# Kernel tuning notes

Measured on AMD Instinct MI355X. Metric: run time of the kernel, lower is better.

The kernel has to match this reference:

```python
import jax, jax.numpy as jnp
import numpy as np

NUM_RELATIONS = 8


def rgcn_conv(x, edge_index, edge_type, W, root, bias):
    """PyG RGCNConv (full weights, aggr='mean'): for each relation r, mean-aggregate
    W_r @ x_src over incoming edges of type r at each target node, sum over relations,
    then add root transform and bias."""
    N = x.shape[0]
    src, dst = edge_index[0], edge_index[1]
    # per-(relation, dst) edge counts for mean aggregation
    comb = edge_type * N + dst  # [E]
    cnt = jax.ops.segment_sum(jnp.ones(src.shape[0], x.dtype), comb,
                              num_segments=NUM_RELATIONS * N)  # [R*N]
    inv = jnp.where(cnt > 0, 1.0 / cnt, 0.0)
    # per-relation transformed features [R, N, H]
    xW = jnp.einsum('ni,rio->rno', x, W)
    # per-edge message, pre-scaled by 1/count for mean aggregation
    msg = xW[edge_type, src] * inv[comb][:, None]  # [E, H]
    agg = jax.ops.segment_sum(msg, dst, num_segments=N)  # [N, H]
    return agg + x @ root + bias


def setup_inputs() -> dict:
    key = jax.random.key(0)
    ks = jax.random.split(key, 9)
    N, E, D, H, C, R = 50000, 600000, 128, 128, 16, NUM_RELATIONS
    s1 = 1.0 / np.sqrt(D)
    s2 = 1.0 / np.sqrt(H)
    return {
        'x': jax.random.normal(ks[0], (N, D), jnp.float32),
        'edge_index': jax.random.randint(ks[1], (2, E), 0, N, jnp.int32),
        'edge_type': jax.random.randint(ks[2], (E,), 0, R, jnp.int32),
        'W1': jax.random.normal(ks[3], (R, D, H), jnp.float32) * s1,
        'root1': jax.random.normal(ks[4], (D, H), jnp.float32) * s1,
        'b1': jnp.zeros((H,), jnp.float32),
        'W2': jax.random.normal(ks[5], (R, H, H), jnp.float32) * s2,
        'root2': jax.random.normal(ks[6], (H, H), jnp.float32) * s2,
        'b2': jnp.zeros((H,), jnp.float32),
        'Wc': jax.random.normal(ks[7], (H, C), jnp.float32) * s2,
        'bc': jnp.zeros((C,), jnp.float32),
    }


def reference(x, edge_index, edge_type, W1, root1, b1, W2, root2, b2, Wc, bc):
    h = jax.nn.relu(rgcn_conv(x, edge_index, edge_type, W1, root1, b1))
    # dropout(p=0.2) is identity in eval mode
    embeddings = rgcn_conv(h, edge_index, edge_type, W2, root2, b2)
    out = embeddings @ Wc + bc
    return (out, embeddings)
```

## Files before the change

kernel.cpp:

```cpp
#include <hip/hip_runtime.h>

#define NREL 8

typedef __attribute__((ext_vector_type(8))) short bf16x8;
typedef __attribute__((ext_vector_type(4))) float f32x4;

__device__ inline ushort f2bf(float f)
{
    union { float f; unsigned u; } v; v.f = f;
    unsigned r = v.u + 0x7FFF + ((v.u >> 16) & 1);
    return (ushort)(r >> 16);
}

__device__ inline unsigned cvtpk(float lo, float hi)
{
    unsigned r;
    asm("v_cvt_pk_bf16_f32 %0, %1, %2" : "=v"(r) : "v"(lo), "v"(hi));
    return r;
}

__global__ __launch_bounds__(256) void prep1(
    float4* __restrict__ cntz, int cnt4,
    const float* __restrict__ x, ushort* __restrict__ xb, int nx4,
    const float* __restrict__ W1, const float* __restrict__ root1,
    ushort* __restrict__ Wf1,
    const float* __restrict__ W2, const float* __restrict__ root2,
    ushort* __restrict__ Wf2)
{
    int tid = blockIdx.x * 256 + threadIdx.x;
    int stride = gridDim.x * 256;

    for (int i = tid; i < cnt4; i += stride)
        cntz[i] = make_float4(0.f, 0.f, 0.f, 0.f);

    for (int i = tid; i < nx4; i += stride) {
        float4 v = ((const float4*)x)[i];
        ushort4 o;
        o.x = f2bf(v.x); o.y = f2bf(v.y); o.z = f2bf(v.z); o.w = f2bf(v.w);
        ((ushort4*)xb)[i] = o;
    }

    const int WFN = 128 * 1152;
    for (int i = tid; i < 2 * WFN; i += stride) {
        int half = (i >= WFN);
        int j = half ? i - WFN : i;
        const float* W    = half ? W2 : W1;
        const float* root = half ? root2 : root1;
        ushort* Wf        = half ? Wf2 : Wf1;
        int f = j >> 9;
        int within = j & 511;
        int l = within >> 3;
        int jj = within & 7;
        int rs = f >> 5;
        int kk = (f >> 3) & 3;
        int n  = f & 7;
        int col = (n << 4) | (l & 15);
        int kl  = kk * 32 + (l >> 4) * 8 + jj;
        float v = (rs < 8) ? W[rs * 16384 + kl * 128 + col]
                           : root[kl * 128 + col];
        Wf[j] = f2bf(v);
    }
}

__global__ __launch_bounds__(256) void count_edges(
    const int* __restrict__ ei, const int* __restrict__ et,
    int* __restrict__ cnt, int E, int N)
{
    int e = blockIdx.x * 256 + threadIdx.x;
    if (e < E) {
        int d = ei[E + e];
        int r = et[e];
        atomicAdd(&cnt[r * N + d], 1);
    }
}

__global__ __launch_bounds__(256) void scan1f(
    const int* __restrict__ cnt, float* __restrict__ invc8,
    int* __restrict__ part, int* __restrict__ bsum, int N)
{
    __shared__ int tmp[256];
    int d = blockIdx.x * 256 + threadIdx.x;
    int s = 0;
    if (d < N) {
        #pragma unroll
        for (int r = 0; r < NREL; r++) {
            int c = cnt[r * N + d];
            s += c;
            invc8[(size_t)d * 8 + r] = (c > 0) ? 1.f / (float)c : 0.f;
        }
    }
    int v = s;
    tmp[threadIdx.x] = v;
    __syncthreads();
    for (int off = 1; off < 256; off <<= 1) {
        int t = (threadIdx.x >= off) ? tmp[threadIdx.x - off] : 0;
        __syncthreads();
        tmp[threadIdx.x] += t;
        __syncthreads();
    }
    if (d < N) part[d] = tmp[threadIdx.x] - v;
    if (threadIdx.x == 255) bsum[blockIdx.x] = tmp[255];
}

__global__ __launch_bounds__(1024) void scan2(int* __restrict__ bsum, int nb)
{
    __shared__ int tmp[1024];
    int tid = threadIdx.x;
    int v = (tid < nb) ? bsum[tid] : 0;
    tmp[tid] = v;
    __syncthreads();
    for (int off = 1; off < 1024; off <<= 1) {
        int t = (tid >= off) ? tmp[tid - off] : 0;
        __syncthreads();
        tmp[tid] += t;
        __syncthreads();
    }
    if (tid < nb) bsum[tid] = tmp[tid] - v;
}

__global__ __launch_bounds__(256) void scan3(
    const int* __restrict__ part, const int* __restrict__ bsum,
    int* __restrict__ rowptr, int* __restrict__ cursor, int n, int E)
{
    int i = blockIdx.x * 256 + threadIdx.x;
    if (i < n) {
        int v = part[i] + bsum[blockIdx.x];
        rowptr[i] = v;
        cursor[i] = v;
    }
    if (i == 0) rowptr[n] = E;
}

__global__ __launch_bounds__(256) void fill_csr(
    const int* __restrict__ ei, const int* __restrict__ et,
    int* __restrict__ cursor, int* __restrict__ spk, int E)
{
    int e = blockIdx.x * 256 + threadIdx.x;
    if (e < E) {
        int d = ei[E + e];
        int pos = atomicAdd(&cursor[d], 1);
        spk[pos] = (ei[e] << 8) | et[e];
    }
}

__global__ __launch_bounds__(1024, 8) void fused_layer(
    const ushort* __restrict__ Xb, const int* __restrict__ rowptr,
    const int* __restrict__ spk, const float* __restrict__ invc8,
    const ushort* __restrict__ Wf, const float* __restrict__ bias,
    float* __restrict__ Ofp, ushort* __restrict__ Obf,
    const float* __restrict__ Wc, const float* __restrict__ bc,
    float* __restrict__ outC, int N, int relu)
{
    __shared__ ushort lds[8 * 32 * 128];
    __shared__ f32x4 pscr[2][512];

    int wid  = threadIdx.x >> 6;
    int lane = threadIdx.x & 63;
    int blk0 = blockIdx.x * 32;
    int lane4 = lane << 2;

    #pragma unroll 1
    for (int rr = 0; rr < 2; rr++) {
        int lrow32 = wid * 2 + rr;
        int d = blk0 + lrow32;

        float2 a0 = {0.f, 0.f}, a1 = {0.f, 0.f}, a2 = {0.f, 0.f}, a3 = {0.f, 0.f};
        float2 a4 = {0.f, 0.f}, a5 = {0.f, 0.f}, a6 = {0.f, 0.f}, a7 = {0.f, 0.f};

        #define ROWLD(SP) \
            (*(const unsigned*)((const char*)Xb + (unsigned)((SP) | lane4)))
        #define CONSUME(P, U)                                               \
        {                                                                   \
            union { unsigned u; float f; } lo, hi;                          \
            lo.u = (U) << 16; hi.u = (U) & 0xFFFF0000u;                     \
            switch ((P) & 0xFF) {                                           \
                case 0: a0.x += lo.f; a0.y += hi.f; break;                  \
                case 1: a1.x += lo.f; a1.y += hi.f; break;                  \
                case 2: a2.x += lo.f; a2.y += hi.f; break;                  \
                case 3: a3.x += lo.f; a3.y += hi.f; break;                  \
                case 4: a4.x += lo.f; a4.y += hi.f; break;                  \
                case 5: a5.x += lo.f; a5.y += hi.f; break;                  \
                case 6: a6.x += lo.f; a6.y += hi.f; break;                  \
                default: a7.x += lo.f; a7.y += hi.f; break;                 \
            }                                                               \
        }

        if (d < N) {
            int beg = rowptr[d], end = rowptr[d + 1];
            int i = beg;
            int pk8 = (i + 8 <= end) ? spk[i + (lane & 7)] : 0;
            for (; i + 8 <= end; ) {
                int cur = pk8;
                i += 8;
                if (i + 8 <= end) pk8 = spk[i + (lane & 7)];
                int p0 = __builtin_amdgcn_readlane(cur, 0);
                int p1 = __builtin_amdgcn_readlane(cur, 1);
                int p2 = __builtin_amdgcn_readlane(cur, 2);
                int p3 = __builtin_amdgcn_readlane(cur, 3);
                int p4 = __builtin_amdgcn_readlane(cur, 4);
                int p5 = __builtin_amdgcn_readlane(cur, 5);
                int p6 = __builtin_amdgcn_readlane(cur, 6);
                int p7 = __builtin_amdgcn_readlane(cur, 7);
                unsigned u0 = ROWLD(p0 & 0xFFFFFF00);
                unsigned u1 = ROWLD(p1 & 0xFFFFFF00);
                unsigned u2 = ROWLD(p2 & 0xFFFFFF00);
                unsigned u3 = ROWLD(p3 & 0xFFFFFF00);
                unsigned u4 = ROWLD(p4 & 0xFFFFFF00);
                unsigned u5 = ROWLD(p5 & 0xFFFFFF00);
                unsigned u6 = ROWLD(p6 & 0xFFFFFF00);
                unsigned u7 = ROWLD(p7 & 0xFFFFFF00);
                CONSUME(p0, u0);
                CONSUME(p1, u1);
                CONSUME(p2, u2);
                CONSUME(p3, u3);
                CONSUME(p4, u4);
                CONSUME(p5, u5);
                CONSUME(p6, u6);
                CONSUME(p7, u7);
            }
            for (; i + 4 <= end; i += 4) {
                int pk4 = spk[i + (lane & 3)];
                int p0 = __builtin_amdgcn_readlane(pk4, 0);
                int p1 = __builtin_amdgcn_readlane(pk4, 1);
                int p2 = __builtin_amdgcn_readlane(pk4, 2);
                int p3 = __builtin_amdgcn_readlane(pk4, 3);
                unsigned u0 = ROWLD(p0 & 0xFFFFFF00);
                unsigned u1 = ROWLD(p1 & 0xFFFFFF00);
                unsigned u2 = ROWLD(p2 & 0xFFFFFF00);
                unsigned u3 = ROWLD(p3 & 0xFFFFFF00);
                CONSUME(p0, u0);
                CONSUME(p1, u1);
                CONSUME(p2, u2);
                CONSUME(p3, u3);
            }
            for (; i < end; i++) {
                int p = __builtin_amdgcn_readfirstlane(spk[i]);
                unsigned u = ROWLD(p & 0xFFFFFF00);
                CONSUME(p, u);
            }
        }
        #undef CONSUME
        #undef ROWLD

        f32x4 iv0 = {0.f, 0.f, 0.f, 0.f}, iv1 = {0.f, 0.f, 0.f, 0.f};
        if (d < N) {
            iv0 = *(const f32x4*)&invc8[(size_t)d * 8];
            iv1 = *(const f32x4*)&invc8[(size_t)d * 8 + 4];
        }
        unsigned swz = (unsigned)(lrow32 & 7) << 4;
        char* rowbase = (char*)lds + (lrow32 << 8);
        unsigned wroff = (((unsigned)lane << 2)) ^ swz;
        #define WR2(R, A, IV)                                               \
        {                                                                   \
            unsigned pk = cvtpk(A.x * (IV), A.y * (IV));                    \
            *(unsigned*)(rowbase + (R << 13) + wroff) = pk;                 \
        }
        WR2(0, a0, iv0[0]) WR2(1, a1, iv0[1]) WR2(2, a2, iv0[2]) WR2(3, a3, iv0[3])
        WR2(4, a4, iv1[0]) WR2(5, a5, iv1[1]) WR2(6, a6, iv1[2]) WR2(7, a7, iv1[3])
        #undef WR2
    }
    __syncthreads();

    int lrow = lane & 15;
    int kgrp = lane >> 4;
    unsigned swzR = (unsigned)(lrow & 7) << 4;
    const bf16x8* Wf8 = (const bf16x8*)Wf;
    int n0    = wid & 7;
    int upper = wid >> 3;

    f32x4 acc0 = {0.f, 0.f, 0.f, 0.f};
    f32x4 acc1 = {0.f, 0.f, 0.f, 0.f};
    const char* ldsb = (const char*)lds;

    int rs0 = upper * 4;
    #pragma unroll 1
    for (int rs = rs0; rs < rs0 + 4; rs++) {
        const bf16x8* Bp = Wf8 + (size_t)rs * 2048 + (size_t)n0 * 64 + lane;
        bf16x8 b0 = Bp[0];
        bf16x8 b1 = Bp[512];
        bf16x8 b2 = Bp[1024];
        bf16x8 b3 = Bp[1536];
        const char* ab0 = ldsb + (rs << 13) + ((0 + lrow) << 8);
        const char* ab1 = ldsb + (rs << 13) + ((16 + lrow) << 8);
        {
            bf16x8 a0 = *(const bf16x8*)(ab0 + ((unsigned)(0 * 64 + kgrp * 16) ^ swzR));
            bf16x8 a1 = *(const bf16x8*)(ab0 + ((unsigned)(1 * 64 + kgrp * 16) ^ swzR));
            bf16x8 a2 = *(const bf16x8*)(ab0 + ((unsigned)(2 * 64 + kgrp * 16) ^ swzR));
            bf16x8 a3 = *(const bf16x8*)(ab0 + ((unsigned)(3 * 64 + kgrp * 16) ^ swzR));
            acc0 = __builtin_amdgcn_mfma_f32_16x16x32_bf16(a0, b0, acc0, 0, 0, 0);
            acc0 = __builtin_amdgcn_mfma_f32_16x16x32_bf16(a1, b1, acc0, 0, 0, 0);
            acc0 = __builtin_amdgcn_mfma_f32_16x16x32_bf16(a2, b2, acc0, 0, 0, 0);
            acc0 = __builtin_amdgcn_mfma_f32_16x16x32_bf16(a3, b3, acc0, 0, 0, 0);
        }
        {
            bf16x8 a0 = *(const bf16x8*)(ab1 + ((unsigned)(0 * 64 + kgrp * 16) ^ swzR));
            bf16x8 a1 = *(const bf16x8*)(ab1 + ((unsigned)(1 * 64 + kgrp * 16) ^ swzR));
            bf16x8 a2 = *(const bf16x8*)(ab1 + ((unsigned)(2 * 64 + kgrp * 16) ^ swzR));
            bf16x8 a3 = *(const bf16x8*)(ab1 + ((unsigned)(3 * 64 + kgrp * 16) ^ swzR));
            acc1 = __builtin_amdgcn_mfma_f32_16x16x32_bf16(a0, b0, acc1, 0, 0, 0);
            acc1 = __builtin_amdgcn_mfma_f32_16x16x32_bf16(a1, b1, acc1, 0, 0, 0);
            acc1 = __builtin_amdgcn_mfma_f32_16x16x32_bf16(a2, b2, acc1, 0, 0, 0);
            acc1 = __builtin_amdgcn_mfma_f32_16x16x32_bf16(a3, b3, acc1, 0, 0, 0);
        }
    }
    {
        int arow0 = blk0 + lrow;      if (arow0 >= N) arow0 = N - 1;
        int arow1 = blk0 + 16 + lrow; if (arow1 >= N) arow1 = N - 1;
        const ushort* A0 = Xb + (size_t)arow0 * 128;
        const ushort* A1 = Xb + (size_t)arow1 * 128;
        const bf16x8* Bp = Wf8 + (size_t)8 * 2048 + (size_t)n0 * 64 + lane;
        int kkb = upper * 2;
        bf16x8 b0 = Bp[(kkb + 0) * 512];
        bf16x8 b1 = Bp[(kkb + 1) * 512];
        bf16x8 a00 = *(const bf16x8*)(A0 + (kkb + 0) * 32 + kgrp * 8);
        bf16x8 a01 = *(const bf16x8*)(A0 + (kkb + 1) * 32 + kgrp * 8);
        bf16x8 a10 = *(const bf16x8*)(A1 + (kkb + 0) * 32 + kgrp * 8);
        bf16x8 a11 = *(const bf16x8*)(A1 + (kkb + 1) * 32 + kgrp * 8);
        acc0 = __builtin_amdgcn_mfma_f32_16x16x32_bf16(a00, b0, acc0, 0, 0, 0);
        acc0 = __builtin_amdgcn_mfma_f32_16x16x32_bf16(a01, b1, acc0, 0, 0, 0);
        acc1 = __builtin_amdgcn_mfma_f32_16x16x32_bf16(a10, b0, acc1, 0, 0, 0);
        acc1 = __builtin_amdgcn_mfma_f32_16x16x32_bf16(a11, b1, acc1, 0, 0, 0);
    }

    if (upper) {
        pscr[0][n0 * 64 + lane] = acc0;
        pscr[1][n0 * 64 + lane] = acc1;
    }
    __syncthreads();

    if (!upper) {
        f32x4 p0 = pscr[0][n0 * 64 + lane];
        f32x4 p1 = pscr[1][n0 * 64 + lane];
        int col = n0 * 16 + lrow;
        float bv = bias[col];
        float* embt = (float*)lds;
        #pragma unroll
        for (int rg = 0; rg < 2; rg++) {
            int lrowb = rg * 16 + kgrp * 4;
            f32x4 a = rg ? acc1 : acc0;
            f32x4 pp = rg ? p1 : p0;
            #pragma unroll
            for (int r = 0; r < 4; r++) {
                int row = blk0 + lrowb + r;
                float v = a[r] + pp[r] + bv;
                if (relu) v = fmaxf(v, 0.f);
                if (outC) embt[(lrowb + r) * 128 + col] = v;
                if (row < N) {
                    if (Ofp) Ofp[(size_t)row * 128 + col] = v;
                    if (Obf) Obf[(size_t)row * 128 + col] = f2bf(v);
                }
            }
        }
    }

    if (outC) {
        __syncthreads();
        int t = threadIdx.x;
        if (t < 512) {
            int row = t >> 4;
            int c = t & 15;
            const float* er = (const float*)lds + row * 128;
            float acc2 = bc[c];
            #pragma unroll 8
            for (int k = 0; k < 128; k++) acc2 += er[k] * Wc[k * 16 + c];
            int grow = blk0 + row;
            if (grow < N) outC[(size_t)grow * 16 + c] = acc2;
        }
    }
}

static inline size_t align256(size_t x) { return (x + 255) & ~(size_t)255; }

extern "C" void kernel_launch(void* const* d_in, const int* in_sizes, int n_in,
                              void* d_out, int out_size, void* d_ws, size_t ws_size,
                              hipStream_t stream)
{
    const float* x     = (const float*)d_in[0];
    const int*   ei    = (const int*)d_in[1];
    const int*   et    = (const int*)d_in[2];
    const float* W1    = (const float*)d_in[3];
    const float* root1 = (const float*)d_in[4];
    const float* b1    = (const float*)d_in[5];
    const float* W2    = (const float*)d_in[6];
    const float* root2 = (const float*)d_in[7];
    const float* b2    = (const float*)d_in[8];
    const float* Wc    = (const float*)d_in[9];
    const float* bc    = (const float*)d_in[10];

    const int N = in_sizes[0] / 128;
    const int E = in_sizes[2];
    const int C = in_sizes[10];

    float* out = (float*)d_out;
    float* emb = out + (size_t)N * C;

    size_t cntB  = align256((size_t)NREL * N * sizeof(int));
    size_t rpB   = align256((size_t)(N + 1) * sizeof(int));
    size_t curB  = align256((size_t)N * sizeof(int));
    size_t bsB   = align256((size_t)1024 * sizeof(int));
    size_t invB  = align256((size_t)N * 8 * sizeof(float));
    size_t spkB  = align256((size_t)E * sizeof(int));
    size_t xbB   = align256((size_t)N * 128 * sizeof(ushort));
    size_t wtB   = align256((size_t)128 * 1152 * sizeof(ushort));

    char* p = (char*)d_ws;
    int*    cnt    = (int*)p;      p += cntB;
    int*    rowptr = (int*)p;      p += rpB;
    int*    cursor = (int*)p;      p += curB;
    int*    part   = (int*)p;      p += curB;
    int*    bsum   = (int*)p;      p += bsB;
    float*  invc8  = (float*)p;    p += invB;
    int*    spk    = (int*)p;      p += spkB;
    ushort* xb     = (ushort*)p;   p += xbB;
    ushort* hb     = (ushort*)p;   p += xbB;
    ushort* Wf1    = (ushort*)p;   p += wtB;
    ushort* Wf2    = (ushort*)p;

    dim3 blk(256);
    int gE    = (E + 255) / 256;
    int gN    = (N + 255) / 256;
    int gFus  = (N + 31) / 32;
    long long cnt4 = (long long)NREL * N / 4;
    int nx4 = N * 32;

    prep1<<<2048, blk, 0, stream>>>((float4*)cnt, (int)cnt4,
                                    x, xb, nx4,
                                    W1, root1, Wf1, W2, root2, Wf2);

    count_edges<<<gE, blk, 0, stream>>>(ei, et, cnt, E, N);
    scan1f<<<gN, blk, 0, stream>>>(cnt, invc8, part, bsum, N);
    scan2<<<1, 1024, 0, stream>>>(bsum, gN);
    scan3<<<gN, blk, 0, stream>>>(part, bsum, rowptr, cursor, N, E);
    fill_csr<<<gE, blk, 0, stream>>>(ei, et, cursor, spk, E);

    fused_layer<<<gFus, dim3(1024), 0, stream>>>(
        xb, rowptr, spk, invc8, Wf1, b1, nullptr, hb,
        nullptr, nullptr, nullptr, N, 1);

    fused_layer<<<gFus, dim3(1024), 0, stream>>>(
        hb, rowptr, spk, invc8, Wf2, b2, emb, nullptr,
        Wc, bc, out, N, 0);
}
```

Before: 236.4 us.

## Sort nodes by in-degree to balance work across waves in fused layer

Builds a degree histogram, scans it, and fills a permutation that groups destination nodes by in-degree. The fused layer kernels process nodes in that permuted order, so the waves within a block see similar edge counts and idle less. The change also drops the software prefetch of the next packed-edge chunk and pads the LDS embedding stride to 132 floats to avoid bank conflicts. In exchange it adds three small kernel launches, an extra indirection per row, and scattered output writes.

New measurement: 570.4 us. 141% more time.

```diff
diff --git a/kernel.cpp b/kernel.cpp
--- a/kernel.cpp
+++ b/kernel.cpp
@@ -20,7 +20,7 @@
 }
 
 __global__ __launch_bounds__(256) void prep1(
-    float4* __restrict__ cntz, int cnt4,
+    float4* __restrict__ cntz, int cnt4, int* __restrict__ hist,
     const float* __restrict__ x, ushort* __restrict__ xb, int nx4,
     const float* __restrict__ W1, const float* __restrict__ root1,
     ushort* __restrict__ Wf1,
@@ -32,6 +32,7 @@
 
     for (int i = tid; i < cnt4; i += stride)
         cntz[i] = make_float4(0.f, 0.f, 0.f, 0.f);
+    if (tid < 512) hist[tid] = 0;
 
     for (int i = tid; i < nx4; i += stride) {
         float4 v = ((const float4*)x)[i];
@@ -143,9 +144,50 @@
     }
 }
 
+__global__ __launch_bounds__(256) void deg_hist(
+    const int* __restrict__ rowptr, int* __restrict__ hist, int N)
+{
+    int d = blockIdx.x * 256 + threadIdx.x;
+    if (d < N) {
+        int deg = rowptr[d + 1] - rowptr[d];
+        if (deg > 511) deg = 511;
+        atomicAdd(&hist[deg], 1);
+    }
+}
+
+__global__ __launch_bounds__(512) void hist_scan(int* __restrict__ hist)
+{
+    __shared__ int tmp[512];
+    int tid = threadIdx.x;
+    int v = hist[tid];
+    tmp[tid] = v;
+    __syncthreads();
+    for (int off = 1; off < 512; off <<= 1) {
+        int t = (tid >= off) ? tmp[tid - off] : 0;
+        __syncthreads();
+        tmp[tid] += t;
+        __syncthreads();
+    }
+    hist[tid] = tmp[tid] - v;
+}
+
+__global__ __launch_bounds__(256) void perm_fill(
+    const int* __restrict__ rowptr, int* __restrict__ bincur,
+    int* __restrict__ perm, int N)
+{
+    int d = blockIdx.x * 256 + threadIdx.x;
+    if (d < N) {
+        int deg = rowptr[d + 1] - rowptr[d];
+        if (deg > 511) deg = 511;
+        int pos = atomicAdd(&bincur[deg], 1);
+        perm[pos] = d;
+    }
+}
+
 __global__ __launch_bounds__(1024, 8) void fused_layer(
     const ushort* __restrict__ Xb, const int* __restrict__ rowptr,
     const int* __restrict__ spk, const float* __restrict__ invc8,
+    const int* __restrict__ perm,
     const ushort* __restrict__ Wf, const float* __restrict__ bias,
     float* __restrict__ Ofp, ushort* __restrict__ Obf,
     const float* __restrict__ Wc, const float* __restrict__ bc,
@@ -162,7 +204,8 @@
     #pragma unroll 1
     for (int rr = 0; rr < 2; rr++) {
         int lrow32 = wid * 2 + rr;
-        int d = blk0 + lrow32;
+        int idx = blk0 + lrow32;
+        int d = (idx < N) ? perm[idx] : -1;
 
         float2 a0 = {0.f, 0.f}, a1 = {0.f, 0.f}, a2 = {0.f, 0.f}, a3 = {0.f, 0.f};
         float2 a4 = {0.f, 0.f}, a5 = {0.f, 0.f}, a6 = {0.f, 0.f}, a7 = {0.f, 0.f};
@@ -185,22 +228,19 @@
             }                                                               \
         }
 
-        if (d < N) {
+        if (d >= 0) {
             int beg = rowptr[d], end = rowptr[d + 1];
             int i = beg;
-            int pk8 = (i + 8 <= end) ? spk[i + (lane & 7)] : 0;
-            for (; i + 8 <= end; ) {
-                int cur = pk8;
-                i += 8;
-                if (i + 8 <= end) pk8 = spk[i + (lane & 7)];
-                int p0 = __builtin_amdgcn_readlane(cur, 0);
-                int p1 = __builtin_amdgcn_readlane(cur, 1);
-                int p2 = __builtin_amdgcn_readlane(cur, 2);
-                int p3 = __builtin_amdgcn_readlane(cur, 3);
-                int p4 = __builtin_amdgcn_readlane(cur, 4);
-                int p5 = __builtin_amdgcn_readlane(cur, 5);
-                int p6 = __builtin_amdgcn_readlane(cur, 6);
-                int p7 = __builtin_amdgcn_readlane(cur, 7);
+            for (; i + 8 <= end; i += 8) {
+                int pk8 = spk[i + (lane & 7)];
+                int p0 = __builtin_amdgcn_readlane(pk8, 0);
+                int p1 = __builtin_amdgcn_readlane(pk8, 1);
+                int p2 = __builtin_amdgcn_readlane(pk8, 2);
+                int p3 = __builtin_amdgcn_readlane(pk8, 3);
+                int p4 = __builtin_amdgcn_readlane(pk8, 4);
+                int p5 = __builtin_amdgcn_readlane(pk8, 5);
+                int p6 = __builtin_amdgcn_readlane(pk8, 6);
+                int p7 = __builtin_amdgcn_readlane(pk8, 7);
                 unsigned u0 = ROWLD(p0 & 0xFFFFFF00);
                 unsigned u1 = ROWLD(p1 & 0xFFFFFF00);
                 unsigned u2 = ROWLD(p2 & 0xFFFFFF00);
@@ -243,7 +283,7 @@
         #undef ROWLD
 
         f32x4 iv0 = {0.f, 0.f, 0.f, 0.f}, iv1 = {0.f, 0.f, 0.f, 0.f};
-        if (d < N) {
+        if (d >= 0) {
             iv0 = *(const f32x4*)&invc8[(size_t)d * 8];
             iv1 = *(const f32x4*)&invc8[(size_t)d * 8 + 4];
         }
@@ -304,8 +344,10 @@
         }
     }
     {
-        int arow0 = blk0 + lrow;      if (arow0 >= N) arow0 = N - 1;
-        int arow1 = blk0 + 16 + lrow; if (arow1 >= N) arow1 = N - 1;
+        int i0 = blk0 + lrow;      if (i0 >= N) i0 = N - 1;
+        int i1 = blk0 + 16 + lrow; if (i1 >= N) i1 = N - 1;
+        int arow0 = perm[i0];
+        int arow1 = perm[i1];
         const ushort* A0 = Xb + (size_t)arow0 * 128;
         const ushort* A1 = Xb + (size_t)arow1 * 128;
         const bf16x8* Bp = Wf8 + (size_t)8 * 2048 + (size_t)n0 * 64 + lane;
@@ -341,11 +383,12 @@
             f32x4 pp = rg ? p1 : p0;
             #pragma unroll
             for (int r = 0; r < 4; r++) {
-                int row = blk0 + lrowb + r;
+                int idx = blk0 + lrowb + r;
                 float v = a[r] + pp[r] + bv;
                 if (relu) v = fmaxf(v, 0.f);
-                if (outC) embt[(lrowb + r) * 128 + col] = v;
-                if (row < N) {
+                if (outC) embt[(lrowb + r) * 132 + col] = v;
+                if (idx < N) {
+                    int row = perm[idx];
                     if (Ofp) Ofp[(size_t)row * 128 + col] = v;
                     if (Obf) Obf[(size_t)row * 128 + col] = f2bf(v);
                 }
@@ -359,12 +402,12 @@
         if (t < 512) {
             int row = t >> 4;
             int c = t & 15;
-            const float* er = (const float*)lds + row * 128;
+            const float* er = (const float*)lds + row * 132;
             float acc2 = bc[c];
             #pragma unroll 8
             for (int k = 0; k < 128; k++) acc2 += er[k] * Wc[k * 16 + c];
-            int grow = blk0 + row;
-            if (grow < N) outC[(size_t)grow * 16 + c] = acc2;
+            int idx = blk0 + row;
+            if (idx < N) outC[(size_t)perm[idx] * 16 + c] = acc2;
         }
     }
 }
@@ -398,6 +441,8 @@
     size_t rpB   = align256((size_t)(N + 1) * sizeof(int));
     size_t curB  = align256((size_t)N * sizeof(int));
     size_t bsB   = align256((size_t)1024 * sizeof(int));
+    size_t hsB   = align256((size_t)512 * sizeof(int));
+    size_t pmB   = align256((size_t)N * sizeof(int));
     size_t invB  = align256((size_t)N * 8 * sizeof(float));
     size_t spkB  = align256((size_t)E * sizeof(int));
     size_t xbB   = align256((size_t)N * 128 * sizeof(ushort));
@@ -409,6 +454,8 @@
     int*    cursor = (int*)p;      p += curB;
     int*    part   = (int*)p;      p += curB;
     int*    bsum   = (int*)p;      p += bsB;
+    int*    hist   = (int*)p;      p += hsB;
+    int*    perm   = (int*)p;      p += pmB;
     float*  invc8  = (float*)p;    p += invB;
     int*    spk    = (int*)p;      p += spkB;
     ushort* xb     = (ushort*)p;   p += xbB;
@@ -423,7 +470,7 @@
     long long cnt4 = (long long)NREL * N / 4;
     int nx4 = N * 32;
 
-    prep1<<<2048, blk, 0, stream>>>((float4*)cnt, (int)cnt4,
+    prep1<<<2048, blk, 0, stream>>>((float4*)cnt, (int)cnt4, hist,
                                     x, xb, nx4,
                                     W1, root1, Wf1, W2, root2, Wf2);
 
@@ -433,11 +480,15 @@
     scan3<<<gN, blk, 0, stream>>>(part, bsum, rowptr, cursor, N, E);
     fill_csr<<<gE, blk, 0, stream>>>(ei, et, cursor, spk, E);
 
+    deg_hist<<<gN, blk, 0, stream>>>(rowptr, hist, N);
+    hist_scan<<<1, 512, 0, stream>>>(hist);
+    perm_fill<<<gN, blk, 0, stream>>>(rowptr, hist, perm, N);
+
     fused_layer<<<gFus, dim3(1024), 0, stream>>>(
-        xb, rowptr, spk, invc8, Wf1, b1, nullptr, hb,
+        xb, rowptr, spk, invc8, perm, Wf1, b1, nullptr, hb,
         nullptr, nullptr, nullptr, N, 1);
 
     fused_layer<<<gFus, dim3(1024), 0, stream>>>(
-        hb, rowptr, spk, invc8, Wf2, b2, emb, nullptr,
+        hb, rowptr, spk, invc8, perm, Wf2, b2, emb, nullptr,
         Wc, bc, out, N, 0);
 }
```
